# Performance work log

Hardware: AMD Instinct MI355X
Metric: run time of the kernel (lower is better)

Reference implementation:

```python
import jax, jax.numpy as jnp
import numpy as np

B, T, F, U, H = 256, 512, 128, 256, 64


def setup_inputs() -> dict:
    key = jax.random.key(0)
    k0, k1, k2, k3, k4 = jax.random.split(key, 5)
    x = jax.random.normal(k0, (B, T, F), dtype=jnp.float32)
    # Keras RandomUniform default range (-0.05, 0.05) for LSTM kernel/bias
    kernel = jax.random.uniform(k1, (F, 4 * U), minval=-0.05, maxval=0.05, dtype=jnp.float32)
    rec_kernel = jax.random.uniform(k2, (U, 4 * U), minval=-0.05, maxval=0.05, dtype=jnp.float32)
    bias = jax.random.uniform(k3, (4 * U,), minval=-0.05, maxval=0.05, dtype=jnp.float32)
    # Dense head: glorot-ish scale for the big [T*U, H] weight
    w_out = jax.random.normal(k4, (T * U, H), dtype=jnp.float32) * (1.0 / np.sqrt(T * U))
    b_out = jnp.zeros((H,), dtype=jnp.float32)
    return {"x": x, "kernel": kernel, "rec_kernel": rec_kernel, "bias": bias,
            "w_out": w_out, "b_out": b_out}


def _lstm_swish(x, kernel, rec_kernel, bias):
    """Keras LSTM with activation=swish, recurrent_activation=sigmoid.
    Gate order along last axis: i, f, c(g), o. Returns full hidden sequence [B,T,U]."""
    b, t, _ = x.shape
    u = rec_kernel.shape[0]
    # Precompute input projections for all timesteps: [B,T,4U]
    xz = jnp.einsum('btf,fg->btg', x, kernel) + bias

    def step(carry, xz_t):
        h, c = carry
        z = xz_t + h @ rec_kernel  # [B,4U]
        zi, zf, zg, zo = jnp.split(z, 4, axis=-1)
        i = jax.nn.sigmoid(zi)
        f = jax.nn.sigmoid(zf)
        g = jax.nn.swish(zg)
        o = jax.nn.sigmoid(zo)
        c_new = f * c + i * g
        h_new = o * jax.nn.swish(c_new)
        return (h_new, c_new), h_new

    h0 = jnp.zeros((b, u), dtype=x.dtype)
    c0 = jnp.zeros((b, u), dtype=x.dtype)
    (_, _), hs = jax.lax.scan(step, (h0, c0), jnp.swapaxes(xz, 0, 1))  # hs: [T,B,U]
    return jnp.swapaxes(hs, 0, 1)  # [B,T,U]


def reference(x, kernel, rec_kernel, bias, w_out, b_out):
    seq = _lstm_swish(x, kernel, rec_kernel, bias)        # [B,T,U]
    flat = seq.reshape(seq.shape[0], -1)                   # [B,T*U]
    return flat @ w_out + b_out                            # [B,horizon]
```

## Files before the change

kernel.cpp:

```cpp
#include <hip/hip_runtime.h>
#include <stdint.h>

#define B_ 256
#define T_ 512
#define F_ 128
#define U_ 256
#define H_ 64
#define G4U (4 * U_)

typedef __attribute__((ext_vector_type(8))) short short8;
typedef __attribute__((ext_vector_type(4))) float f32x4;
typedef __attribute__((ext_vector_type(4))) uint32_t u32x4;
typedef unsigned long long ull;

#define BARRIER_LDS() asm volatile("s_waitcnt lgkmcnt(0)\ns_barrier" ::: "memory")

__device__ __forceinline__ uint16_t f2bf(float f) {
  uint32_t u = __builtin_bit_cast(uint32_t, f);
  u += 0x7fffu + ((u >> 16) & 1u);
  return (uint16_t)(u >> 16);
}
__device__ __forceinline__ float sigm(float z) {
  return 1.0f / (1.0f + __expf(-z));
}
__device__ __forceinline__ ull ald(const ull* p) {
  return __hip_atomic_load(p, __ATOMIC_RELAXED, __HIP_MEMORY_SCOPE_AGENT);
}

__global__ __launch_bounds__(256, 1) void lstm_kernel(
    const float* __restrict__ x, const float* __restrict__ kern,
    const float* __restrict__ rker, const float* __restrict__ bias,
    uint16_t* __restrict__ seq, ull* __restrict__ hbuf)
{
  const int tid  = threadIdx.x;
  const int lane = tid & 63;
  const int wv   = tid >> 6;
  const int bg   = blockIdx.x & 15;
  const int ug   = blockIdx.x >> 4;

  __shared__ __align__(16) uint16_t x_stage[4][64][8];
  __shared__ __align__(16) uint16_t h_stage[8][64][8];
  __shared__ __align__(16) float    z_stage[128][20];

  short8 wf[2][8];
  short8 kf[2][4];
  float  bias_r[2];
  #pragma unroll
  for (int i2 = 0; i2 < 2; ++i2) {
    const int ct   = wv * 2 + i2;
    const int cloc = ct * 16 + (lane & 15);
    const int gcol = (cloc >> 5) * U_ + ug * 32 + (cloc & 31);
    bias_r[i2] = bias[gcol];
    #pragma unroll
    for (int kt = 0; kt < 8; ++kt) {
      short8 v;
      #pragma unroll
      for (int j = 0; j < 8; ++j) {
        const int k = kt * 32 + (lane >> 4) * 8 + j;
        v[j] = (short)f2bf(rker[(size_t)k * G4U + gcol]);
      }
      wf[i2][kt] = v;
    }
    #pragma unroll
    for (int kt = 0; kt < 4; ++kt) {
      short8 v;
      #pragma unroll
      for (int j = 0; j < 8; ++j) {
        const int k = kt * 32 + (lane >> 4) * 8 + j;
        v[j] = (short)f2bf(kern[(size_t)k * G4U + gcol]);
      }
      kf[i2][kt] = v;
    }
  }

  const int xrow = tid & 15;
  const int xfb  = (tid >> 6) * 32 + ((tid >> 4) & 3) * 8;
  const int gr  = tid & 15;
  const int u0  = (tid >> 4) * 2;
  const int erow = lane & 15;
  const int ec0  = (tid >> 6) * 16 + ((lane >> 4) & 3) * 4;

  float cst0 = 0.f, cst1 = 0.f;

  float xp[8];
  {
    const float* p = x + ((size_t)(bg * 16 + xrow) * T_ + 0) * F_ + xfb;
    #pragma unroll
    for (int j = 0; j < 8; ++j) xp[j] = p[j];
    uint16_t* d = (uint16_t*)x_stage + tid * 8;
    #pragma unroll
    for (int j = 0; j < 8; ++j) d[j] = f2bf(xp[j]);
  }
  __syncthreads();

  for (int t = 0; t < T_; ++t) {
    f32x4 acc0 = {bias_r[0], bias_r[0], bias_r[0], bias_r[0]};
    f32x4 acc1 = {bias_r[1], bias_r[1], bias_r[1], bias_r[1]};
    #pragma unroll
    for (int kt = 0; kt < 4; ++kt) {
      short8 a = *(const short8*)&x_stage[kt][lane][0];
      acc0 = __builtin_amdgcn_mfma_f32_16x16x32_bf16(a, kf[0][kt], acc0, 0, 0, 0);
      acc1 = __builtin_amdgcn_mfma_f32_16x16x32_bf16(a, kf[1][kt], acc1, 0, 0, 0);
    }
    {
      const int tn = (t + 1 < T_) ? t + 1 : t;
      const float* p = x + ((size_t)(bg * 16 + xrow) * T_ + tn) * F_ + xfb;
      #pragma unroll
      for (int j = 0; j < 8; ++j) xp[j] = p[j];
    }
    if (t > 0) {
      const uint32_t expt = (uint32_t)t;
      const ull* sb = hbuf + (size_t)((t - 1) & 1) * (B_ * 128)
                           + (size_t)(bg * 16 + erow) * 128;
      const ull* pa = sb + ec0;
      const ull* pb = sb + ec0 + 64;
      ull v0, v1, v2, v3, w0, w1, w2, w3;
      for (;;) {
        v0 = ald(pa + 0); v1 = ald(pa + 1); v2 = ald(pa + 2); v3 = ald(pa + 3);
        w0 = ald(pb + 0); w1 = ald(pb + 1); w2 = ald(pb + 2); w3 = ald(pb + 3);
        uint32_t bad = ((uint32_t)(v0 >> 32) ^ expt) | ((uint32_t)(v1 >> 32) ^ expt)
                     | ((uint32_t)(v2 >> 32) ^ expt) | ((uint32_t)(v3 >> 32) ^ expt)
                     | ((uint32_t)(w0 >> 32) ^ expt) | ((uint32_t)(w1 >> 32) ^ expt)
                     | ((uint32_t)(w2 >> 32) ^ expt) | ((uint32_t)(w3 >> 32) ^ expt);
        if (bad == 0u) break;
      }
      u32x4* hs = (u32x4*)h_stage;
      hs[tid]       = (u32x4){(uint32_t)v0, (uint32_t)v1, (uint32_t)v2, (uint32_t)v3};
      hs[tid + 256] = (u32x4){(uint32_t)w0, (uint32_t)w1, (uint32_t)w2, (uint32_t)w3};
    }
    BARRIER_LDS();
    if (t > 0) {
      #pragma unroll
      for (int kt = 0; kt < 8; ++kt) {
        short8 a = *(const short8*)&h_stage[kt][lane][0];
        acc0 = __builtin_amdgcn_mfma_f32_16x16x32_bf16(a, wf[0][kt], acc0, 0, 0, 0);
        acc1 = __builtin_amdgcn_mfma_f32_16x16x32_bf16(a, wf[1][kt], acc1, 0, 0, 0);
      }
    }
    {
      const int c0 = (wv * 2 + 0) * 16 + (lane & 15);
      const int c1 = (wv * 2 + 1) * 16 + (lane & 15);
      const int r0 = (lane >> 4) * 4;
      *(f32x4*)&z_stage[c0][r0] = acc0;
      *(f32x4*)&z_stage[c1][r0] = acc1;
      uint16_t* d = (uint16_t*)x_stage + tid * 8;
      #pragma unroll
      for (int j = 0; j < 8; ++j) d[j] = f2bf(xp[j]);
    }
    BARRIER_LDS();
    {
      const float zi0 = z_stage[u0][gr],      zi1 = z_stage[u0 + 1][gr];
      const float zf0 = z_stage[32 + u0][gr], zf1 = z_stage[33 + u0][gr];
      const float zg0 = z_stage[64 + u0][gr], zg1 = z_stage[65 + u0][gr];
      const float zo0 = z_stage[96 + u0][gr], zo1 = z_stage[97 + u0][gr];
      const float i0 = sigm(zi0), i1 = sigm(zi1);
      const float f0 = sigm(zf0), f1 = sigm(zf1);
      const float g0 = zg0 * sigm(zg0), g1 = zg1 * sigm(zg1);
      const float o0 = sigm(zo0), o1 = sigm(zo1);
      cst0 = f0 * cst0 + i0 * g0;
      cst1 = f1 * cst1 + i1 * g1;
      const float h0 = o0 * (cst0 * sigm(cst0));
      const float h1 = o1 * (cst1 * sigm(cst1));
      const uint32_t packed = (uint32_t)f2bf(h0) | ((uint32_t)f2bf(h1) << 16);
      ull* wp = hbuf + (size_t)(t & 1) * (B_ * 128)
                     + (size_t)(bg * 16 + gr) * 128 + ((ug * 32 + u0) >> 1);
      __hip_atomic_store(wp, (ull)packed | ((ull)(uint32_t)(t + 1) << 32),
                         __ATOMIC_RELAXED, __HIP_MEMORY_SCOPE_AGENT);
      *(uint32_t*)(seq + ((size_t)(bg * 16 + gr) * T_ + t) * U_ + ug * 32 + u0) = packed;
    }
  }
}

__global__ __launch_bounds__(256, 1) void head_kernel(
    const uint16_t* __restrict__ seq, const float* __restrict__ w_out,
    float* __restrict__ partials)
{
  const int g    = blockIdx.x;
  const int tid  = threadIdx.x;
  const int lane = tid & 63;
  const int wv   = tid >> 6;

  f32x4 acc[4][4];
  #pragma unroll
  for (int i = 0; i < 4; ++i)
    #pragma unroll
    for (int c = 0; c < 4; ++c) acc[i][c] = (f32x4){0.f, 0.f, 0.f, 0.f};

  for (int ks = 0; ks < 64; ++ks) {
    const int krow = g * 2048 + ks * 32 + (lane >> 4) * 8;
    short8 bf[4];
    #pragma unroll
    for (int c = 0; c < 4; ++c) {
      short8 v;
      #pragma unroll
      for (int j = 0; j < 8; ++j)
        v[j] = (short)f2bf(w_out[(size_t)(krow + j) * H_ + c * 16 + (lane & 15)]);
      bf[c] = v;
    }
    #pragma unroll
    for (int i = 0; i < 4; ++i) {
      const int b = (wv * 4 + i) * 16 + (lane & 15);
      short8 a = *(const short8*)(seq + (size_t)b * (T_ * U_) + krow);
      #pragma unroll
      for (int c = 0; c < 4; ++c)
        acc[i][c] = __builtin_amdgcn_mfma_f32_16x16x32_bf16(a, bf[c], acc[i][c], 0, 0, 0);
    }
  }
  #pragma unroll
  for (int i = 0; i < 4; ++i)
    #pragma unroll
    for (int c = 0; c < 4; ++c)
      #pragma unroll
      for (int r = 0; r < 4; ++r) {
        const int b = wv * 64 + i * 16 + (lane >> 4) * 4 + r;
        partials[((size_t)g * B_ + b) * H_ + c * 16 + (lane & 15)] = acc[i][c][r];
      }
}

__global__ void reduce_kernel(const float* __restrict__ partials,
                              const float* __restrict__ b_out,
                              float* __restrict__ out)
{
  const int i = blockIdx.x * 256 + threadIdx.x;
  float s = b_out[i & (H_ - 1)];
  #pragma unroll 8
  for (int g = 0; g < 64; ++g) s += partials[(size_t)g * (B_ * H_) + i];
  out[i] = s;
}

extern "C" void kernel_launch(void* const* d_in, const int* in_sizes, int n_in,
                              void* d_out, int out_size, void* d_ws, size_t ws_size,
                              hipStream_t stream) {
  (void)in_sizes; (void)n_in; (void)out_size; (void)ws_size;
  const float* x     = (const float*)d_in[0];
  const float* kern  = (const float*)d_in[1];
  const float* rker  = (const float*)d_in[2];
  const float* bias  = (const float*)d_in[3];
  const float* w_out = (const float*)d_in[4];
  const float* b_out = (const float*)d_in[5];
  float* out = (float*)d_out;

  char* ws = (char*)d_ws;
  const size_t seq_bytes  = (size_t)B_ * T_ * U_ * 2;
  const size_t hbuf_bytes = (size_t)2 * B_ * 128 * 8;
  uint16_t* seq      = (uint16_t*)ws;
  ull*      hbuf     = (ull*)(ws + seq_bytes);
  float*    partials = (float*)(ws + seq_bytes + hbuf_bytes);

  hipMemsetAsync(hbuf, 0, hbuf_bytes, stream);

  lstm_kernel<<<128, 256, 0, stream>>>(x, kern, rker, bias, seq, hbuf);
  head_kernel<<<64, 256, 0, stream>>>(seq, w_out, partials);
  reduce_kernel<<<64, 256, 0, stream>>>(partials, b_out, out);
}
```

Baseline: 1.477 ms.

## Repartition LSTM recurrence to two blocks per batch group with register gates

The recurrent LSTM kernel drops from 128 to 32 blocks. Each block now owns 128 hidden units with all four gates, so gate math runs directly on the MFMA accumulators without a z_stage LDS round-trip or an extra barrier. Each step only exchanges half of h with a single peer block through flag-tagged global stores, and the local half is written straight into a double-buffered LDS stage. This cuts per-step cross-block sync traffic and LDS passes, but raises register pressure (4x the weight fragments per thread) and leaves fewer CUs doing the serial work.

```diff
diff --git a/kernel.cpp b/kernel.cpp
--- a/kernel.cpp
+++ b/kernel.cpp
@@ -10,7 +10,6 @@
 
 typedef __attribute__((ext_vector_type(8))) short short8;
 typedef __attribute__((ext_vector_type(4))) float f32x4;
-typedef __attribute__((ext_vector_type(4))) uint32_t u32x4;
 typedef unsigned long long ull;
 
 #define BARRIER_LDS() asm volatile("s_waitcnt lgkmcnt(0)\ns_barrier" ::: "memory")
@@ -35,52 +34,57 @@
   const int tid  = threadIdx.x;
   const int lane = tid & 63;
   const int wv   = tid >> 6;
+  const int il   = lane & 15;
+  const int rg   = lane >> 4;
   const int bg   = blockIdx.x & 15;
-  const int ug   = blockIdx.x >> 4;
+  const int m    = blockIdx.x >> 4;
 
   __shared__ __align__(16) uint16_t x_stage[4][64][8];
-  __shared__ __align__(16) uint16_t h_stage[8][64][8];
-  __shared__ __align__(16) float    z_stage[128][20];
-
-  short8 wf[2][8];
-  short8 kf[2][4];
-  float  bias_r[2];
-  #pragma unroll
-  for (int i2 = 0; i2 < 2; ++i2) {
-    const int ct   = wv * 2 + i2;
-    const int cloc = ct * 16 + (lane & 15);
-    const int gcol = (cloc >> 5) * U_ + ug * 32 + (cloc & 31);
-    bias_r[i2] = bias[gcol];
-    #pragma unroll
-    for (int kt = 0; kt < 8; ++kt) {
-      short8 v;
-      #pragma unroll
-      for (int j = 0; j < 8; ++j) {
-        const int k = kt * 32 + (lane >> 4) * 8 + j;
-        v[j] = (short)f2bf(rker[(size_t)k * G4U + gcol]);
-      }
-      wf[i2][kt] = v;
-    }
-    #pragma unroll
-    for (int kt = 0; kt < 4; ++kt) {
-      short8 v;
-      #pragma unroll
-      for (int j = 0; j < 8; ++j) {
-        const int k = kt * 32 + (lane >> 4) * 8 + j;
-        v[j] = (short)f2bf(kern[(size_t)k * G4U + gcol]);
-      }
-      kf[i2][kt] = v;
-    }
-  }
+  __shared__ __align__(16) uint16_t h_stage[2][8][64][8];
+
+  short8 wf[4][2][8];
+  short8 kf[4][2][4];
+  float  bias_r[4][2];
+  #pragma unroll
+  for (int q = 0; q < 4; ++q)
+    #pragma unroll
+    for (int d = 0; d < 2; ++d) {
+      const int ul   = (wv * 2 + d) * 16 + il;
+      const int gcol = q * U_ + m * 128 + ul;
+      bias_r[q][d] = bias[gcol];
+      #pragma unroll
+      for (int kt = 0; kt < 8; ++kt) {
+        short8 v;
+        #pragma unroll
+        for (int j = 0; j < 8; ++j)
+          v[j] = (short)f2bf(rker[(size_t)(kt * 32 + rg * 8 + j) * G4U + gcol]);
+        wf[q][d][kt] = v;
+      }
+      #pragma unroll
+      for (int kt = 0; kt < 4; ++kt) {
+        short8 v;
+        #pragma unroll
+        for (int j = 0; j < 8; ++j)
+          v[j] = (short)f2bf(kern[(size_t)(kt * 32 + rg * 8 + j) * G4U + gcol]);
+        kf[q][d][kt] = v;
+      }
+    }
 
   const int xrow = tid & 15;
   const int xfb  = (tid >> 6) * 32 + ((tid >> 4) & 3) * 8;
-  const int gr  = tid & 15;
-  const int u0  = (tid >> 4) * 2;
-  const int erow = lane & 15;
-  const int ec0  = (tid >> 6) * 16 + ((lane >> 4) & 3) * 4;
-
-  float cst0 = 0.f, cst1 = 0.f;
+
+  const int Ua = m * 128 + wv * 32 + il;
+  const int kta = Ua >> 5, posa = Ua & 7, ga = ((Ua & 31) >> 3) * 16;
+  const int posb = (Ua + 16) & 7, gb = (((Ua + 16) & 31) >> 3) * 16;
+
+  ull* const pub   = hbuf + ((size_t)(bg * 2 + m) * 2) * 1024;
+  const ull* const peer = hbuf + ((size_t)(bg * 2 + (1 - m)) * 2) * 1024;
+
+  float cst[2][4];
+  #pragma unroll
+  for (int d = 0; d < 2; ++d)
+    #pragma unroll
+    for (int j = 0; j < 4; ++j) cst[d][j] = 0.f;
 
   float xp[8];
   {
@@ -94,13 +98,26 @@
   __syncthreads();
 
   for (int t = 0; t < T_; ++t) {
-    f32x4 acc0 = {bias_r[0], bias_r[0], bias_r[0], bias_r[0]};
-    f32x4 acc1 = {bias_r[1], bias_r[1], bias_r[1], bias_r[1]};
+    ull pv[4];
+    const ull* pp = peer + (size_t)((t - 1) & 1) * 1024 + tid * 4;
+    if (t > 0) {
+      #pragma unroll
+      for (int k = 0; k < 4; ++k) pv[k] = ald(pp + k);
+    }
+    f32x4 acc[4][2];
+    #pragma unroll
+    for (int q = 0; q < 4; ++q)
+      #pragma unroll
+      for (int d = 0; d < 2; ++d)
+        acc[q][d] = (f32x4){bias_r[q][d], bias_r[q][d], bias_r[q][d], bias_r[q][d]};
     #pragma unroll
     for (int kt = 0; kt < 4; ++kt) {
       short8 a = *(const short8*)&x_stage[kt][lane][0];
-      acc0 = __builtin_amdgcn_mfma_f32_16x16x32_bf16(a, kf[0][kt], acc0, 0, 0, 0);
-      acc1 = __builtin_amdgcn_mfma_f32_16x16x32_bf16(a, kf[1][kt], acc1, 0, 0, 0);
+      #pragma unroll
+      for (int q = 0; q < 4; ++q)
+        #pragma unroll
+        for (int d = 0; d < 2; ++d)
+          acc[q][d] = __builtin_amdgcn_mfma_f32_16x16x32_bf16(a, kf[q][d][kt], acc[q][d], 0, 0, 0);
     }
     {
       const int tn = (t + 1 < T_) ? t + 1 : t;
@@ -110,64 +127,71 @@
     }
     if (t > 0) {
       const uint32_t expt = (uint32_t)t;
-      const ull* sb = hbuf + (size_t)((t - 1) & 1) * (B_ * 128)
-                           + (size_t)(bg * 16 + erow) * 128;
-      const ull* pa = sb + ec0;
-      const ull* pb = sb + ec0 + 64;
-      ull v0, v1, v2, v3, w0, w1, w2, w3;
       for (;;) {
-        v0 = ald(pa + 0); v1 = ald(pa + 1); v2 = ald(pa + 2); v3 = ald(pa + 3);
-        w0 = ald(pb + 0); w1 = ald(pb + 1); w2 = ald(pb + 2); w3 = ald(pb + 3);
-        uint32_t bad = ((uint32_t)(v0 >> 32) ^ expt) | ((uint32_t)(v1 >> 32) ^ expt)
-                     | ((uint32_t)(v2 >> 32) ^ expt) | ((uint32_t)(v3 >> 32) ^ expt)
-                     | ((uint32_t)(w0 >> 32) ^ expt) | ((uint32_t)(w1 >> 32) ^ expt)
-                     | ((uint32_t)(w2 >> 32) ^ expt) | ((uint32_t)(w3 >> 32) ^ expt);
-        if (bad == 0u) break;
-      }
-      u32x4* hs = (u32x4*)h_stage;
-      hs[tid]       = (u32x4){(uint32_t)v0, (uint32_t)v1, (uint32_t)v2, (uint32_t)v3};
-      hs[tid + 256] = (u32x4){(uint32_t)w0, (uint32_t)w1, (uint32_t)w2, (uint32_t)w3};
+        bool ok = ((uint32_t)(pv[0] >> 32) == expt) & ((uint32_t)(pv[1] >> 32) == expt)
+                & ((uint32_t)(pv[2] >> 32) == expt) & ((uint32_t)(pv[3] >> 32) == expt);
+        if (ok) break;
+        #pragma unroll
+        for (int k = 0; k < 4; ++k) pv[k] = ald(pp + k);
+      }
+      const int ss = (t - 1) & 1;
+      const int r  = tid >> 4;
+      #pragma unroll
+      for (int k = 0; k < 4; ++k) {
+        const int q  = (tid & 15) * 4 + k;
+        const int Up = (1 - m) * 128 + (q >> 4) * 32 + (q & 15);
+        const int Uq = Up + 16;
+        h_stage[ss][Up >> 5][(((Up & 31) >> 3) * 16) + r][Up & 7] = (uint16_t)pv[k];
+        h_stage[ss][Uq >> 5][(((Uq & 31) >> 3) * 16) + r][Uq & 7] = (uint16_t)(pv[k] >> 16);
+      }
     }
     BARRIER_LDS();
     if (t > 0) {
+      const int ss = (t - 1) & 1;
       #pragma unroll
       for (int kt = 0; kt < 8; ++kt) {
-        short8 a = *(const short8*)&h_stage[kt][lane][0];
-        acc0 = __builtin_amdgcn_mfma_f32_16x16x32_bf16(a, wf[0][kt], acc0, 0, 0, 0);
-        acc1 = __builtin_amdgcn_mfma_f32_16x16x32_bf16(a, wf[1][kt], acc1, 0, 0, 0);
-      }
-    }
+        short8 a = *(const short8*)&h_stage[ss][kt][lane][0];
+        #pragma unroll
+        for (int q = 0; q < 4; ++q)
+          #pragma unroll
+          for (int d = 0; d < 2; ++d)
+            acc[q][d] = __builtin_amdgcn_mfma_f32_16x16x32_bf16(a, wf[q][d][kt], acc[q][d], 0, 0, 0);
+      }
+    }
+    float hh[2][4];
+    #pragma unroll
+    for (int d = 0; d < 2; ++d)
+      #pragma unroll
+      for (int j = 0; j < 4; ++j) {
+        const float zi = acc[0][d][j], zf = acc[1][d][j];
+        const float zg = acc[2][d][j], zo = acc[3][d][j];
+        const float ii = sigm(zi), ff = sigm(zf);
+        const float gg = zg * sigm(zg), oo = sigm(zo);
+        const float c  = ff * cst[d][j] + ii * gg;
+        cst[d][j] = c;
+        hh[d][j]  = oo * (c * sigm(c));
+      }
     {
-      const int c0 = (wv * 2 + 0) * 16 + (lane & 15);
-      const int c1 = (wv * 2 + 1) * 16 + (lane & 15);
-      const int r0 = (lane >> 4) * 4;
-      *(f32x4*)&z_stage[c0][r0] = acc0;
-      *(f32x4*)&z_stage[c1][r0] = acc1;
-      uint16_t* d = (uint16_t*)x_stage + tid * 8;
-      #pragma unroll
-      for (int j = 0; j < 8; ++j) d[j] = f2bf(xp[j]);
+      const int s2 = t & 1;
+      ull* pw = pub + (size_t)s2 * 1024;
+      #pragma unroll
+      for (int j = 0; j < 4; ++j) {
+        const int r = rg * 4 + j;
+        const uint16_t b0 = f2bf(hh[0][j]), b1 = f2bf(hh[1][j]);
+        const uint32_t packed = (uint32_t)b0 | ((uint32_t)b1 << 16);
+        __hip_atomic_store(pw + (r * 64 + wv * 16 + il),
+                           (ull)packed | ((ull)(uint32_t)(t + 1) << 32),
+                           __ATOMIC_RELAXED, __HIP_MEMORY_SCOPE_AGENT);
+        h_stage[s2][kta][ga + r][posa] = b0;
+        h_stage[s2][kta][gb + r][posb] = b1;
+        uint16_t* sp = seq + ((size_t)(bg * 16 + r) * T_ + t) * U_;
+        sp[Ua] = b0; sp[Ua + 16] = b1;
+      }
+      uint16_t* xd = (uint16_t*)x_stage + tid * 8;
+      #pragma unroll
+      for (int j = 0; j < 8; ++j) xd[j] = f2bf(xp[j]);
     }
     BARRIER_LDS();
-    {
-      const float zi0 = z_stage[u0][gr],      zi1 = z_stage[u0 + 1][gr];
-      const float zf0 = z_stage[32 + u0][gr], zf1 = z_stage[33 + u0][gr];
-      const float zg0 = z_stage[64 + u0][gr], zg1 = z_stage[65 + u0][gr];
-      const float zo0 = z_stage[96 + u0][gr], zo1 = z_stage[97 + u0][gr];
-      const float i0 = sigm(zi0), i1 = sigm(zi1);
-      const float f0 = sigm(zf0), f1 = sigm(zf1);
-      const float g0 = zg0 * sigm(zg0), g1 = zg1 * sigm(zg1);
-      const float o0 = sigm(zo0), o1 = sigm(zo1);
-      cst0 = f0 * cst0 + i0 * g0;
-      cst1 = f1 * cst1 + i1 * g1;
-      const float h0 = o0 * (cst0 * sigm(cst0));
-      const float h1 = o1 * (cst1 * sigm(cst1));
-      const uint32_t packed = (uint32_t)f2bf(h0) | ((uint32_t)f2bf(h1) << 16);
-      ull* wp = hbuf + (size_t)(t & 1) * (B_ * 128)
-                     + (size_t)(bg * 16 + gr) * 128 + ((ug * 32 + u0) >> 1);
-      __hip_atomic_store(wp, (ull)packed | ((ull)(uint32_t)(t + 1) << 32),
-                         __ATOMIC_RELAXED, __HIP_MEMORY_SCOPE_AGENT);
-      *(uint32_t*)(seq + ((size_t)(bg * 16 + gr) * T_ + t) * U_ + ug * 32 + u0) = packed;
-    }
   }
 }
 
@@ -242,14 +266,14 @@
 
   char* ws = (char*)d_ws;
   const size_t seq_bytes  = (size_t)B_ * T_ * U_ * 2;
-  const size_t hbuf_bytes = (size_t)2 * B_ * 128 * 8;
+  const size_t hbuf_bytes = (size_t)16 * 2 * 2 * 1024 * 8;
   uint16_t* seq      = (uint16_t*)ws;
   ull*      hbuf     = (ull*)(ws + seq_bytes);
   float*    partials = (float*)(ws + seq_bytes + hbuf_bytes);
 
   hipMemsetAsync(hbuf, 0, hbuf_bytes, stream);
 
-  lstm_kernel<<<128, 256, 0, stream>>>(x, kern, rker, bias, seq, hbuf);
+  lstm_kernel<<<32, 256, 0, stream>>>(x, kern, rker, bias, seq, hbuf);
   head_kernel<<<64, 256, 0, stream>>>(seq, w_out, partials);
   reduce_kernel<<<64, 256, 0, stream>>>(partials, b_out, out);
 }
```

After: 2.811 ms. +90.3%, slower.
